# Performance work log

Measured on AMD Instinct MI355X. Metric: run time of the kernel, lower is better.

## Reference

```python
import jax, jax.numpy as jnp
import numpy as np

N_NODES = 50000
N_EDGES = 800000
IN_DIM = 128
HIDDEN = 128
OUT_DIM = 40


def setup_inputs() -> dict:
    key = jax.random.key(0)
    ks = jax.random.split(key, 6)
    x = jax.random.normal(ks[0], (N_NODES, IN_DIM), dtype=jnp.float32)
    edge_src = jax.random.randint(ks[1], (N_EDGES,), 0, N_NODES, dtype=jnp.int32)
    edge_dst = jax.random.randint(ks[2], (N_EDGES,), 0, N_NODES, dtype=jnp.int32)
    edge_weight = jax.random.uniform(ks[3], (N_EDGES,), dtype=jnp.float32)
    W1 = jax.random.normal(ks[4], (IN_DIM, HIDDEN), dtype=jnp.float32) / np.sqrt(IN_DIM)
    b1 = jnp.zeros((HIDDEN,), dtype=jnp.float32)
    W2 = jax.random.normal(ks[5], (HIDDEN, OUT_DIM), dtype=jnp.float32) / np.sqrt(HIDDEN)
    b2 = jnp.zeros((OUT_DIM,), dtype=jnp.float32)
    return {"x": x, "edge_src": edge_src, "edge_dst": edge_dst,
            "edge_weight": edge_weight, "W1": W1, "b1": b1, "W2": W2, "b2": b2}


def _spmm(edge_src, edge_dst, edge_weight, x):
    # out[i] = sum_{e: dst==i} w_e * x[src_e]   (sparse adj @ x)
    msgs = edge_weight[:, None] * x[edge_src]  # [E, D] gather
    return jax.ops.segment_sum(msgs, edge_dst, num_segments=N_NODES)


def reference(x, edge_src, edge_dst, edge_weight, W1, b1, W2, b2):
    # dropout p=0.0 (eval): identity
    h = _spmm(edge_src, edge_dst, edge_weight, x)       # adj @ x
    h = jax.nn.relu(h @ W1 + b1)                        # lin1 + relu
    h = _spmm(edge_src, edge_dst, edge_weight, h)       # adj @ h
    return h @ W2 + b2                                  # lin2
```

## Files before the change

kernel.cpp:

```cpp
#include <hip/hip_runtime.h>
#include <hip/hip_bf16.h>

#define N_NODES 50000
#define N_EDGES 800000
#define IN_DIM 128
#define HIDDEN 128
#define OUT_DIM 40
#define G_STRIDE 64

#define SCAN_BS 1024
#define SCAN_BLOCKS ((N_NODES + SCAN_BS - 1) / SCAN_BS)

#define N_COPIES 8
#define HIST_STRIDE 50176

#define HIST_BLOCKS 3128
#define G1_BLOCKS ((N_NODES + 63) / 64)
#define HG_GRID 3910

struct __align__(8) Edge { int s; float w; };

typedef __attribute__((ext_vector_type(8))) short bf16x8;
typedef __attribute__((ext_vector_type(4))) float f32x4;
typedef __attribute__((ext_vector_type(8))) unsigned short u16x8;
typedef __attribute__((ext_vector_type(4))) unsigned short u16x4;

__device__ __forceinline__ unsigned f32_to_bf16_bits(float f) {
    unsigned u = __float_as_uint(f);
    return (u + 0x7FFFu + ((u >> 16) & 1u)) >> 16;
}
__device__ __forceinline__ float b2f(unsigned short u) {
    return __uint_as_float(((unsigned)u) << 16);
}
__device__ __forceinline__ int src_slice(int s) {
    return (int)((unsigned)s / 6250u);
}

__global__ __launch_bounds__(256) void hist_gemm1(const int* __restrict__ dst,
                                                  const int* __restrict__ srcv,
                                                  int* __restrict__ hist8,
                                                  unsigned short* __restrict__ erank,
                                                  const float* __restrict__ x,
                                                  const float* __restrict__ W1,
                                                  __hip_bfloat16* __restrict__ y)
{
    __shared__ bf16x8 w1s[2048];
    int bid = blockIdx.x;

    if ((bid % 5) != 4) {
        int hb = bid - bid / 5;
        int i = hb * 256 + threadIdx.x;
        if (i < N_EDGES) {
            int copy = src_slice(srcv[i]);
            erank[i] = (unsigned short)atomicAdd(&hist8[copy * HIST_STRIDE + dst[i]], 1);
        }
        return;
    }

    int gb = bid / 5;
    int t = threadIdx.x;
    for (int f = t; f < 2048; f += 256) {
        int lane = f & 63;
        int nt = (f >> 6) & 7;
        int ks = f >> 9;
        int m = lane & 15, quad = lane >> 4;
        bf16x8 frag;
        #pragma unroll
        for (int j = 0; j < 8; ++j) {
            int k = ks * 32 + quad * 8 + j;
            frag[j] = (short)f32_to_bf16_bits(W1[k * HIDDEN + nt * 16 + m]);
        }
        w1s[f] = frag;
    }
    __syncthreads();

    int wv = t >> 6;
    int lane = t & 63;
    int m = lane & 15, quad = lane >> 4;
    int row0 = gb * 64 + wv * 16;
    int arow = row0 + m;
    if (arow >= N_NODES) arow = N_NODES - 1;

    bf16x8 afrag[4];
    #pragma unroll
    for (int ks = 0; ks < 4; ++ks) {
        const float4* xp = (const float4*)(x + (long long)arow * IN_DIM + ks * 32 + quad * 8);
        float4 a0 = xp[0], a1 = xp[1];
        afrag[ks][0] = (short)f32_to_bf16_bits(a0.x);
        afrag[ks][1] = (short)f32_to_bf16_bits(a0.y);
        afrag[ks][2] = (short)f32_to_bf16_bits(a0.z);
        afrag[ks][3] = (short)f32_to_bf16_bits(a0.w);
        afrag[ks][4] = (short)f32_to_bf16_bits(a1.x);
        afrag[ks][5] = (short)f32_to_bf16_bits(a1.y);
        afrag[ks][6] = (short)f32_to_bf16_bits(a1.z);
        afrag[ks][7] = (short)f32_to_bf16_bits(a1.w);
    }

    f32x4 acc[8];
    #pragma unroll
    for (int nt = 0; nt < 8; ++nt) acc[nt] = (f32x4){0.f, 0.f, 0.f, 0.f};

    #pragma unroll
    for (int ks = 0; ks < 4; ++ks) {
        #pragma unroll
        for (int nt = 0; nt < 8; ++nt) {
            bf16x8 bfrag = w1s[(ks * 8 + nt) * 64 + lane];
            acc[nt] = __builtin_amdgcn_mfma_f32_16x16x32_bf16(afrag[ks], bfrag, acc[nt], 0, 0, 0);
        }
    }

    #pragma unroll
    for (int nt = 0; nt < 8; ++nt) {
        #pragma unroll
        for (int r = 0; r < 4; ++r) {
            int rrow = row0 + quad * 4 + r;
            if (rrow < N_NODES)
                y[(long long)rrow * HIDDEN + nt * 16 + m] = __float2bfloat16(acc[nt][r]);
        }
    }
}

__global__ __launch_bounds__(SCAN_BS) void scan_partial(int* __restrict__ hist8,
                                                        int* __restrict__ cnt,
                                                        int* __restrict__ block_sums)
{
    __shared__ int red[SCAN_BS / 64];
    int i = blockIdx.x * SCAN_BS + threadIdx.x;
    int total = 0;
    if (i < N_NODES) {
        int off = 0;
        #pragma unroll
        for (int c = 0; c < N_COPIES; ++c) {
            int h = hist8[c * HIST_STRIDE + i];
            hist8[c * HIST_STRIDE + i] = off;
            off += h;
        }
        total = off;
        cnt[i] = total;
    }
    int s = total;
    for (int off = 32; off > 0; off >>= 1) s += __shfl_down(s, off, 64);
    int wave = threadIdx.x >> 6, lane = threadIdx.x & 63;
    if (lane == 0) red[wave] = s;
    __syncthreads();
    if (threadIdx.x == 0) {
        int tt = 0;
        #pragma unroll
        for (int wv = 0; wv < SCAN_BS / 64; ++wv) tt += red[wv];
        block_sums[blockIdx.x] = tt;
    }
}

__global__ __launch_bounds__(SCAN_BS) void scan_final(const int* __restrict__ cnt,
                                                      const int* __restrict__ block_sums,
                                                      int* __restrict__ row_ptr)
{
    __shared__ int tmp[SCAN_BS];
    __shared__ int blk_off;
    int t = threadIdx.x;
    int i = blockIdx.x * SCAN_BS + t;
    if (t < 64) {
        int v2 = (t < (int)blockIdx.x) ? block_sums[t] : 0;
        for (int off = 32; off > 0; off >>= 1) v2 += __shfl_down(v2, off, 64);
        if (t == 0) {
            blk_off = v2;
            if (blockIdx.x == 0) row_ptr[N_NODES] = N_EDGES;
        }
    }
    int v = (i < N_NODES) ? cnt[i] : 0;
    tmp[t] = v;
    __syncthreads();
    for (int off = 1; off < SCAN_BS; off <<= 1) {
        int u = (t >= off) ? tmp[t - off] : 0;
        __syncthreads();
        tmp[t] += u;
        __syncthreads();
    }
    if (i < N_NODES) row_ptr[i] = tmp[t] - v + blk_off;
}

__global__ __launch_bounds__(256) void scatter_det(const int* __restrict__ src,
                                                   const int* __restrict__ dst,
                                                   const float* __restrict__ w,
                                                   const int* __restrict__ hist8,
                                                   const unsigned short* __restrict__ erank,
                                                   const int* __restrict__ row_ptr,
                                                   Edge* __restrict__ edges)
{
    int i = blockIdx.x * 256 + threadIdx.x;
    int d = dst[i];
    int s = src[i];
    int copy = src_slice(s);
    int pos = row_ptr[d] + hist8[copy * HIST_STRIDE + d] + (int)erank[i];
    Edge ed; ed.s = s; ed.w = w[i];
    edges[pos] = ed;
}

__global__ __launch_bounds__(256) void spmm1_kernel(const int* __restrict__ row_ptr,
                                                    const Edge* __restrict__ edges,
                                                    const __hip_bfloat16* __restrict__ y,
                                                    const float* __restrict__ b1,
                                                    __hip_bfloat16* __restrict__ h1)
{
    int wv = threadIdx.x >> 6;
    int lane = threadIdx.x & 63;
    int grp = lane >> 4;
    int sub = lane & 15;
    int node = blockIdx.x * 16 + wv * 4 + grp;
    int j = row_ptr[node];
    int e = row_ptr[node + 1];

    float acc[8];
    #pragma unroll
    for (int k = 0; k < 8; ++k) acc[k] = 0.f;

    for (; j + 7 < e; j += 8) {
        Edge ed[8];
        #pragma unroll
        for (int u = 0; u < 8; ++u) ed[u] = edges[j + u];
        u16x8 v[8];
        #pragma unroll
        for (int u = 0; u < 8; ++u)
            v[u] = *(const u16x8*)(y + ((long long)ed[u].s << 7) + (sub << 3));
        #pragma unroll
        for (int u = 0; u < 8; ++u) {
            #pragma unroll
            for (int k = 0; k < 8; ++k)
                acc[k] = fmaf(ed[u].w, b2f(v[u][k]), acc[k]);
        }
    }
    for (; j + 3 < e; j += 4) {
        Edge ed[4];
        #pragma unroll
        for (int u = 0; u < 4; ++u) ed[u] = edges[j + u];
        u16x8 v[4];
        #pragma unroll
        for (int u = 0; u < 4; ++u)
            v[u] = *(const u16x8*)(y + ((long long)ed[u].s << 7) + (sub << 3));
        #pragma unroll
        for (int u = 0; u < 4; ++u) {
            #pragma unroll
            for (int k = 0; k < 8; ++k)
                acc[k] = fmaf(ed[u].w, b2f(v[u][k]), acc[k]);
        }
    }
    for (; j < e; ++j) {
        Edge ed0 = edges[j];
        u16x8 v0 = *(const u16x8*)(y + ((long long)ed0.s << 7) + (sub << 3));
        #pragma unroll
        for (int k = 0; k < 8; ++k)
            acc[k] = fmaf(ed0.w, b2f(v0[k]), acc[k]);
    }

    float4 bA = *(const float4*)(b1 + (sub << 3));
    float4 bB = *(const float4*)(b1 + (sub << 3) + 4);
    u16x8 hv;
    hv[0] = (unsigned short)f32_to_bf16_bits(fmaxf(acc[0] + bA.x, 0.f));
    hv[1] = (unsigned short)f32_to_bf16_bits(fmaxf(acc[1] + bA.y, 0.f));
    hv[2] = (unsigned short)f32_to_bf16_bits(fmaxf(acc[2] + bA.z, 0.f));
    hv[3] = (unsigned short)f32_to_bf16_bits(fmaxf(acc[3] + bA.w, 0.f));
    hv[4] = (unsigned short)f32_to_bf16_bits(fmaxf(acc[4] + bB.x, 0.f));
    hv[5] = (unsigned short)f32_to_bf16_bits(fmaxf(acc[5] + bB.y, 0.f));
    hv[6] = (unsigned short)f32_to_bf16_bits(fmaxf(acc[6] + bB.z, 0.f));
    hv[7] = (unsigned short)f32_to_bf16_bits(fmaxf(acc[7] + bB.w, 0.f));
    *(u16x8*)(h1 + ((long long)node << 7) + (sub << 3)) = hv;
}

#define G2_ROWS 8
__global__ __launch_bounds__(64) void gemm2_kernel(const __hip_bfloat16* __restrict__ h1,
                                                   const float* __restrict__ W2,
                                                   __hip_bfloat16* __restrict__ g)
{
    __shared__ float xs[G2_ROWS][HIDDEN];
    int row0 = blockIdx.x * G2_ROWS;
    int t = threadIdx.x;
    #pragma unroll
    for (int r = 0; r < G2_ROWS; ++r) {
        xs[r][t]      = __bfloat162float(h1[(long long)(row0 + r) * HIDDEN + t]);
        xs[r][t + 64] = __bfloat162float(h1[(long long)(row0 + r) * HIDDEN + t + 64]);
    }
    __syncthreads();
    if (t >= OUT_DIM) {
        __hip_bfloat16 z = __float2bfloat16(0.f);
        #pragma unroll
        for (int r = 0; r < G2_ROWS; ++r)
            g[((row0 + r) << 6) + t] = z;
        return;
    }
    float acc[G2_ROWS];
    #pragma unroll
    for (int r = 0; r < G2_ROWS; ++r) acc[r] = 0.f;
    #pragma unroll 4
    for (int k = 0; k < HIDDEN; ++k) {
        float wv = W2[k * OUT_DIM + t];
        #pragma unroll
        for (int r = 0; r < G2_ROWS; ++r)
            acc[r] = fmaf(xs[r][k], wv, acc[r]);
    }
    #pragma unroll
    for (int r = 0; r < G2_ROWS; ++r)
        g[((row0 + r) << 6) + t] = __float2bfloat16(acc[r]);
}

__global__ __launch_bounds__(256) void spmm2_kernel(const int* __restrict__ row_ptr,
                                                    const Edge* __restrict__ edges,
                                                    const __hip_bfloat16* __restrict__ g,
                                                    const float* __restrict__ b2,
                                                    float* __restrict__ out)
{
    int wv = threadIdx.x >> 6;
    int lane = threadIdx.x & 63;
    int grp = lane >> 4;
    int sub = lane & 15;
    int node = blockIdx.x * 16 + wv * 4 + grp;
    int j = row_ptr[node];
    int e = row_ptr[node + 1];

    float acc[4];
    #pragma unroll
    for (int k = 0; k < 4; ++k) acc[k] = 0.f;

    for (; j + 7 < e; j += 8) {
        Edge ed[8];
        #pragma unroll
        for (int u = 0; u < 8; ++u) ed[u] = edges[j + u];
        u16x4 v[8];
        #pragma unroll
        for (int u = 0; u < 8; ++u)
            v[u] = *(const u16x4*)(g + ((long long)ed[u].s << 6) + (sub << 2));
        #pragma unroll
        for (int u = 0; u < 8; ++u) {
            #pragma unroll
            for (int k = 0; k < 4; ++k)
                acc[k] = fmaf(ed[u].w, b2f(v[u][k]), acc[k]);
        }
    }
    for (; j + 3 < e; j += 4) {
        Edge ed[4];
        #pragma unroll
        for (int u = 0; u < 4; ++u) ed[u] = edges[j + u];
        u16x4 v[4];
        #pragma unroll
        for (int u = 0; u < 4; ++u)
            v[u] = *(const u16x4*)(g + ((long long)ed[u].s << 6) + (sub << 2));
        #pragma unroll
        for (int u = 0; u < 4; ++u) {
            #pragma unroll
            for (int k = 0; k < 4; ++k)
                acc[k] = fmaf(ed[u].w, b2f(v[u][k]), acc[k]);
        }
    }
    for (; j < e; ++j) {
        Edge ed0 = edges[j];
        u16x4 v0 = *(const u16x4*)(g + ((long long)ed0.s << 6) + (sub << 2));
        #pragma unroll
        for (int k = 0; k < 4; ++k)
            acc[k] = fmaf(ed0.w, b2f(v0[k]), acc[k]);
    }

    if (sub < 10) {
        float4 bb = *(const float4*)(b2 + (sub << 2));
        float4 o;
        o.x = acc[0] + bb.x;
        o.y = acc[1] + bb.y;
        o.z = acc[2] + bb.z;
        o.w = acc[3] + bb.w;
        *(float4*)(out + (long long)node * OUT_DIM + (sub << 2)) = o;
    }
}

extern "C" void kernel_launch(void* const* d_in, const int* in_sizes, int n_in,
                              void* d_out, int out_size, void* d_ws, size_t ws_size,
                              hipStream_t stream)
{
    const float* x    = (const float*)d_in[0];
    const int*   esrc = (const int*)  d_in[1];
    const int*   edst = (const int*)  d_in[2];
    const float* ew   = (const float*)d_in[3];
    const float* W1   = (const float*)d_in[4];
    const float* b1   = (const float*)d_in[5];
    const float* W2   = (const float*)d_in[6];
    const float* b2   = (const float*)d_in[7];
    float* out = (float*)d_out;

    __hip_bfloat16* y  = (__hip_bfloat16*)d_ws;
    __hip_bfloat16* g  = y;
    __hip_bfloat16* h1 = y + (size_t)N_NODES * HIDDEN;
    Edge* edges     = (Edge*)(h1 + (size_t)N_NODES * HIDDEN);
    int* hist8      = (int*)(edges + N_EDGES);
    unsigned short* erank = (unsigned short*)(hist8 + N_COPIES * HIST_STRIDE);
    int* cnt        = (int*)(erank + N_EDGES);
    int* row_ptr    = cnt + 50176;
    int* block_sums = row_ptr + 50176;

    hipMemsetAsync(hist8, 0, N_COPIES * HIST_STRIDE * sizeof(int), stream);
    hist_gemm1<<<HG_GRID, 256, 0, stream>>>(edst, esrc, hist8, erank, x, W1, y);
    scan_partial<<<SCAN_BLOCKS, SCAN_BS, 0, stream>>>(hist8, cnt, block_sums);
    scan_final<<<SCAN_BLOCKS, SCAN_BS, 0, stream>>>(cnt, block_sums, row_ptr);
    scatter_det<<<N_EDGES / 256, 256, 0, stream>>>(esrc, edst, ew, hist8,
                                                   erank, row_ptr, edges);

    spmm1_kernel<<<N_NODES / 16, 256, 0, stream>>>(row_ptr, edges, y, b1, h1);
    gemm2_kernel<<<N_NODES / G2_ROWS, 64, 0, stream>>>(h1, W2, g);
    spmm2_kernel<<<N_NODES / 16, 256, 0, stream>>>(row_ptr, edges, g, b2, out);
}
```

Before: 216.6 us.

## Fuse two-pass scan with decoupled lookback and move gemm2 to MFMA

The two scan kernels become one: each block publishes its total as a flag in spare hist8 slots (past node 50000) with release/acquire atomics, and later blocks spin on earlier flags, which removes one launch and the cnt/block_sums round trips. The scalar gemm2 kernel (64 threads, 8 rows per block) is replaced by a bf16 MFMA 16x16x32 kernel that builds W2 fragments in LDS and zero-pads the output columns from 40 to 64. The spin-wait relies on all 49 scan blocks being co-resident, which holds on this GPU, and it reuses hist8 entries that were zeroed by the memset.

```diff
diff --git a/kernel.cpp b/kernel.cpp
--- a/kernel.cpp
+++ b/kernel.cpp
@@ -13,6 +13,7 @@
 
 #define N_COPIES 8
 #define HIST_STRIDE 50176
+#define FLAG_BASE 50000
 
 #define HIST_BLOCKS 3128
 #define G1_BLOCKS ((N_NODES + 63) / 64)
@@ -120,12 +121,16 @@
     }
 }
 
-__global__ __launch_bounds__(SCAN_BS) void scan_partial(int* __restrict__ hist8,
-                                                        int* __restrict__ cnt,
-                                                        int* __restrict__ block_sums)
-{
+__global__ __launch_bounds__(SCAN_BS) void scan_fused(int* __restrict__ hist8,
+                                                      int* __restrict__ row_ptr)
+{
+    __shared__ int tmp[SCAN_BS];
     __shared__ int red[SCAN_BS / 64];
-    int i = blockIdx.x * SCAN_BS + threadIdx.x;
+    __shared__ int blk_off;
+    int t = threadIdx.x;
+    int bid = blockIdx.x;
+    int i = bid * SCAN_BS + t;
+
     int total = 0;
     if (i < N_NODES) {
         int off = 0;
@@ -136,38 +141,36 @@
             off += h;
         }
         total = off;
-        cnt[i] = total;
     }
     int s = total;
     for (int off = 32; off > 0; off >>= 1) s += __shfl_down(s, off, 64);
-    int wave = threadIdx.x >> 6, lane = threadIdx.x & 63;
+    int wave = t >> 6, lane = t & 63;
     if (lane == 0) red[wave] = s;
     __syncthreads();
-    if (threadIdx.x == 0) {
+    if (t == 0) {
         int tt = 0;
         #pragma unroll
         for (int wv = 0; wv < SCAN_BS / 64; ++wv) tt += red[wv];
-        block_sums[blockIdx.x] = tt;
-    }
-}
-
-__global__ __launch_bounds__(SCAN_BS) void scan_final(const int* __restrict__ cnt,
-                                                      const int* __restrict__ block_sums,
-                                                      int* __restrict__ row_ptr)
-{
-    __shared__ int tmp[SCAN_BS];
-    __shared__ int blk_off;
-    int t = threadIdx.x;
-    int i = blockIdx.x * SCAN_BS + t;
+        __hip_atomic_store(&hist8[FLAG_BASE + bid], tt + 1,
+                           __ATOMIC_RELEASE, __HIP_MEMORY_SCOPE_AGENT);
+    }
     if (t < 64) {
-        int v2 = (t < (int)blockIdx.x) ? block_sums[t] : 0;
+        int v2 = 0;
+        if (t < bid) {
+            int v;
+            do {
+                v = __hip_atomic_load(&hist8[FLAG_BASE + t],
+                                      __ATOMIC_ACQUIRE, __HIP_MEMORY_SCOPE_AGENT);
+            } while (v == 0);
+            v2 = v - 1;
+        }
         for (int off = 32; off > 0; off >>= 1) v2 += __shfl_down(v2, off, 64);
         if (t == 0) {
             blk_off = v2;
-            if (blockIdx.x == 0) row_ptr[N_NODES] = N_EDGES;
-        }
-    }
-    int v = (i < N_NODES) ? cnt[i] : 0;
+            if (bid == 0) row_ptr[N_NODES] = N_EDGES;
+        }
+    }
+    int v = total;
     tmp[t] = v;
     __syncthreads();
     for (int off = 1; off < SCAN_BS; off <<= 1) {
@@ -266,40 +269,75 @@
     *(u16x8*)(h1 + ((long long)node << 7) + (sub << 3)) = hv;
 }
 
-#define G2_ROWS 8
-__global__ __launch_bounds__(64) void gemm2_kernel(const __hip_bfloat16* __restrict__ h1,
-                                                   const float* __restrict__ W2,
-                                                   __hip_bfloat16* __restrict__ g)
-{
-    __shared__ float xs[G2_ROWS][HIDDEN];
-    int row0 = blockIdx.x * G2_ROWS;
+__global__ __launch_bounds__(256) void gemm2_mfma(const __hip_bfloat16* __restrict__ h1,
+                                                  const float* __restrict__ W2,
+                                                  __hip_bfloat16* __restrict__ g)
+{
+    __shared__ bf16x8 w2s[768];
     int t = threadIdx.x;
-    #pragma unroll
-    for (int r = 0; r < G2_ROWS; ++r) {
-        xs[r][t]      = __bfloat162float(h1[(long long)(row0 + r) * HIDDEN + t]);
-        xs[r][t + 64] = __bfloat162float(h1[(long long)(row0 + r) * HIDDEN + t + 64]);
+    for (int f = t; f < 768; f += 256) {
+        int lane = f & 63;
+        int nt = (f >> 6) % 3;
+        int ks = f / 192;
+        int m = lane & 15, quad = lane >> 4;
+        int col = nt * 16 + m;
+        bf16x8 frag;
+        #pragma unroll
+        for (int j = 0; j < 8; ++j) {
+            int k = ks * 32 + quad * 8 + j;
+            float val = (col < OUT_DIM) ? W2[k * OUT_DIM + col] : 0.f;
+            frag[j] = (short)f32_to_bf16_bits(val);
+        }
+        w2s[f] = frag;
     }
     __syncthreads();
-    if (t >= OUT_DIM) {
-        __hip_bfloat16 z = __float2bfloat16(0.f);
-        #pragma unroll
-        for (int r = 0; r < G2_ROWS; ++r)
-            g[((row0 + r) << 6) + t] = z;
-        return;
-    }
-    float acc[G2_ROWS];
-    #pragma unroll
-    for (int r = 0; r < G2_ROWS; ++r) acc[r] = 0.f;
-    #pragma unroll 4
-    for (int k = 0; k < HIDDEN; ++k) {
-        float wv = W2[k * OUT_DIM + t];
-        #pragma unroll
-        for (int r = 0; r < G2_ROWS; ++r)
-            acc[r] = fmaf(xs[r][k], wv, acc[r]);
-    }
-    #pragma unroll
-    for (int r = 0; r < G2_ROWS; ++r)
-        g[((row0 + r) << 6) + t] = __float2bfloat16(acc[r]);
+
+    int wv = t >> 6;
+    int lane = t & 63;
+    int m = lane & 15, quad = lane >> 4;
+    int row0 = blockIdx.x * 64 + wv * 16;
+    int arow = row0 + m;
+    if (arow >= N_NODES) arow = N_NODES - 1;
+
+    bf16x8 afrag[4];
+    #pragma unroll
+    for (int ks = 0; ks < 4; ++ks)
+        afrag[ks] = *(const bf16x8*)(h1 + (long long)arow * HIDDEN + ks * 32 + quad * 8);
+
+    f32x4 acc[3];
+    #pragma unroll
+    for (int nt = 0; nt < 3; ++nt) acc[nt] = (f32x4){0.f, 0.f, 0.f, 0.f};
+
+    #pragma unroll
+    for (int ks = 0; ks < 4; ++ks) {
+        #pragma unroll
+        for (int nt = 0; nt < 3; ++nt) {
+            bf16x8 bfrag = w2s[(ks * 3 + nt) * 64 + lane];
+            acc[nt] = __builtin_amdgcn_mfma_f32_16x16x32_bf16(afrag[ks], bfrag, acc[nt], 0, 0, 0);
+        }
+    }
+
+    #pragma unroll
+    for (int nt = 0; nt < 3; ++nt) {
+        int col = nt * 16 + m;
+        if (col < OUT_DIM) {
+            #pragma unroll
+            for (int r = 0; r < 4; ++r) {
+                int rrow = row0 + quad * 4 + r;
+                if (rrow < N_NODES)
+                    g[(rrow << 6) + col] = __float2bfloat16(acc[nt][r]);
+            }
+        }
+    }
+    if (m < 6) {
+        u16x4 z = (u16x4){0, 0, 0, 0};
+        #pragma unroll
+        for (int r = 0; r < 4; ++r) {
+            int rrow = row0 + quad * 4 + r;
+            if (rrow < N_NODES)
+                *(u16x4*)(g + (rrow << 6) + OUT_DIM + m * 4) = z;
+        }
+    }
 }
 
 __global__ __launch_bounds__(256) void spmm2_kernel(const int* __restrict__ row_ptr,
@@ -389,18 +427,15 @@
     Edge* edges     = (Edge*)(h1 + (size_t)N_NODES * HIDDEN);
     int* hist8      = (int*)(edges + N_EDGES);
     unsigned short* erank = (unsigned short*)(hist8 + N_COPIES * HIST_STRIDE);
-    int* cnt        = (int*)(erank + N_EDGES);
-    int* row_ptr    = cnt + 50176;
-    int* block_sums = row_ptr + 50176;
+    int* row_ptr    = (int*)(erank + N_EDGES);
 
     hipMemsetAsync(hist8, 0, N_COPIES * HIST_STRIDE * sizeof(int), stream);
     hist_gemm1<<<HG_GRID, 256, 0, stream>>>(edst, esrc, hist8, erank, x, W1, y);
-    scan_partial<<<SCAN_BLOCKS, SCAN_BS, 0, stream>>>(hist8, cnt, block_sums);
-    scan_final<<<SCAN_BLOCKS, SCAN_BS, 0, stream>>>(cnt, block_sums, row_ptr);
+    scan_fused<<<SCAN_BLOCKS, SCAN_BS, 0, stream>>>(hist8, row_ptr);
     scatter_det<<<N_EDGES / 256, 256, 0, stream>>>(esrc, edst, ew, hist8,
                                                    erank, row_ptr, edges);
 
     spmm1_kernel<<<N_NODES / 16, 256, 0, stream>>>(row_ptr, edges, y, b1, h1);
-    gemm2_kernel<<<N_NODES / G2_ROWS, 64, 0, stream>>>(h1, W2, g);
+    gemm2_mfma<<<G1_BLOCKS, 256, 0, stream>>>(h1, W2, g);
     spmm2_kernel<<<N_NODES / 16, 256, 0, stream>>>(row_ptr, edges, g, b2, out);
 }
```

Result: faster. 202.1 us (-6.7%).
